# Optimization experiments

Hardware: AMD Instinct MI355X
Metric: run time of the kernel (lower is better)

Reference implementation:

```python
import jax, jax.numpy as jnp
import numpy as np

N_TREES = 10
N_DEPTH = 8
IN_DIM = 2048
CLASSES = 1000
BATCH = 16384
N_DECISION = 2 ** N_DEPTH - 1          # 255
N_LEAF = 2 ** (N_DEPTH + 1)            # 512 (module's own convention)


def _tiling_pattern():
    # Static gather pattern mapping each (leaf, depth) slot to an index into
    # the packed [decision_p, 1 - decision_p] tensor, exactly as in the source.
    tp = np.zeros((N_LEAF, N_DEPTH), dtype=np.int32)
    dec_idx = 0
    for n in range(N_DEPTH):
        j = 0
        for _ in range(2 ** n):
            rep = 2 ** (N_DEPTH - n)
            tp[j:j + rep, n] = dec_idx
            j += rep
            tp[j:j + rep, n] = N_DECISION + dec_idx
            j += rep
            dec_idx += 1
    return tp.reshape(-1)

FLAT_PATTERN = jnp.asarray(_tiling_pattern())  # [N_LEAF * N_DEPTH]


def setup_inputs() -> dict:
    key = jax.random.key(0)
    kx, kd, kl = jax.random.split(key, 3)
    x = jax.random.normal(kx, (BATCH, IN_DIM), dtype=jnp.float32)
    # small scale so sigmoid logits are not fully saturated (mimics uniform init)
    w_d = jax.random.normal(kd, (N_TREES, IN_DIM, N_DECISION), dtype=jnp.float32) * 0.02
    w_l = jax.random.normal(kl, (N_TREES, N_LEAF, CLASSES), dtype=jnp.float32)
    return {"x": x, "w_d": w_d, "w_l": w_l}


def reference(x, w_d, w_l):
    # decision probabilities for all trees: [T, B, N_DECISION]
    decision_p = jax.nn.sigmoid(jnp.einsum('bi,tid->tbd', x, w_d))
    # packed [p, 1-p]: [T, B, 2*N_DECISION]
    pack = jnp.concatenate([decision_p, 1.0 - decision_p], axis=-1)
    # static gather -> path probability factors: [T, B, N_LEAF, N_DEPTH]
    mu = pack[..., FLAT_PATTERN].reshape(N_TREES, x.shape[0], N_LEAF, N_DEPTH)
    leaf_prob = jnp.prod(mu, axis=-1)               # [T, B, N_LEAF]
    leaf_p = jax.nn.softmax(w_l, axis=-1)           # [T, N_LEAF, C]
    # sum over trees, then average
    return jnp.einsum('tbl,tlc->bc', leaf_prob, leaf_p) / N_TREES
```

## Files before the change

### kernel.cpp

```cpp
#include <hip/hip_runtime.h>
#include <stdint.h>

#define T_TREES 10
#define IN_DIM  2048
#define BATCH   16384
#define CLASSES 1000
#define NDEC    255
#define NPAD    256
#define K2DIM   (T_TREES * NPAD)
#define NPADC   1024

typedef unsigned short u16;
typedef float floatx4 __attribute__((ext_vector_type(4)));
typedef __bf16 bf16x8 __attribute__((ext_vector_type(8)));

__device__ __forceinline__ u16 f2bf(float f) {
    union { float f; uint32_t u; } v; v.f = f;
    uint32_t u = v.u;
    return (u16)((u + 0x7FFFu + ((u >> 16) & 1u)) >> 16);
}
__device__ __forceinline__ float bf2f(u16 h) {
    union { uint32_t u; float f; } v; v.u = ((uint32_t)h) << 16;
    return v.f;
}

__device__ __forceinline__ void gld16(u16* lds, const u16* g) {
    __builtin_amdgcn_global_load_lds(
        (__attribute__((address_space(1))) const void*)g,
        (__attribute__((address_space(3))) void*)lds,
        16, 0, 0);
}

__global__ __launch_bounds__(256) void cast_x_k(const float4* __restrict__ x,
                                                uint2* __restrict__ xb) {
    int i = blockIdx.x * 256 + threadIdx.x;
    float4 v = x[i];
    uint2 o;
    o.x = (uint32_t)f2bf(v.x) | ((uint32_t)f2bf(v.y) << 16);
    o.y = (uint32_t)f2bf(v.z) | ((uint32_t)f2bf(v.w) << 16);
    xb[i] = o;
}

__global__ void transpose_wd_k(const float* __restrict__ wd, u16* __restrict__ wdT) {
    __shared__ float tile[32][33];
    int tx = threadIdx.x, ty = threadIdx.y;
    int t = blockIdx.z;
    int i0 = blockIdx.x * 32, d0 = blockIdx.y * 32;
#pragma unroll
    for (int r = 0; r < 4; ++r) {
        int i = i0 + ty + r * 8;
        int d = d0 + tx;
        float v = (d < NDEC) ? wd[((size_t)t * IN_DIM + i) * NDEC + d] : 0.0f;
        tile[ty + r * 8][tx] = v;
    }
    __syncthreads();
#pragma unroll
    for (int r = 0; r < 4; ++r) {
        int dd = d0 + ty + r * 8;
        int ii = i0 + tx;
        wdT[((size_t)t * NPAD + dd) * IN_DIM + ii] = f2bf(tile[tx][ty + r * 8]);
    }
}

__global__ __launch_bounds__(256) void softmax_fold_k(const float* __restrict__ wl,
                                                      u16* __restrict__ B2) {
    int wid = threadIdx.x >> 6, lane = threadIdx.x & 63;
    int idx = blockIdx.x * 4 + wid;
    int t = idx >> 8, m = idx & 255;
    const float* r0 = wl + ((size_t)t * 512 + 2 * m) * CLASSES;
    const float* r1 = r0 + CLASSES;
    float v0[16], v1[16];
    float mx0 = -3.0e38f, mx1 = -3.0e38f;
#pragma unroll
    for (int j = 0; j < 16; ++j) {
        int c = lane + 64 * j;
        float a = (c < CLASSES) ? r0[c] : -3.0e38f;
        float b = (c < CLASSES) ? r1[c] : -3.0e38f;
        v0[j] = a; v1[j] = b;
        mx0 = fmaxf(mx0, a); mx1 = fmaxf(mx1, b);
    }
#pragma unroll
    for (int o = 32; o > 0; o >>= 1) {
        mx0 = fmaxf(mx0, __shfl_xor(mx0, o));
        mx1 = fmaxf(mx1, __shfl_xor(mx1, o));
    }
    float s0 = 0.f, s1 = 0.f;
#pragma unroll
    for (int j = 0; j < 16; ++j) {
        int c = lane + 64 * j;
        float e0 = (c < CLASSES) ? __expf(v0[j] - mx0) : 0.f;
        float e1 = (c < CLASSES) ? __expf(v1[j] - mx1) : 0.f;
        v0[j] = e0; v1[j] = e1; s0 += e0; s1 += e1;
    }
#pragma unroll
    for (int o = 32; o > 0; o >>= 1) { s0 += __shfl_xor(s0, o); s1 += __shfl_xor(s1, o); }
    float i0 = 0.1f / s0, i1 = 0.1f / s1;
#pragma unroll
    for (int j = 0; j < 16; ++j) {
        int c = lane + 64 * j;
        float v = (c < CLASSES) ? (v0[j] * i0 + v1[j] * i1) : 0.f;
        B2[(size_t)idx * NPADC + c] = f2bf(v);
    }
}

__global__ void transpose_b2_k(const u16* __restrict__ B2, u16* __restrict__ B2t) {
    __shared__ u16 tile[32][33];
    int tx = threadIdx.x, ty = threadIdx.y;
    int k0 = blockIdx.x * 32, c0 = blockIdx.y * 32;
#pragma unroll
    for (int r = 0; r < 4; ++r)
        tile[ty + r * 8][tx] = B2[(size_t)(k0 + ty + r * 8) * NPADC + c0 + tx];
    __syncthreads();
#pragma unroll
    for (int r = 0; r < 4; ++r)
        B2t[(size_t)(c0 + ty + r * 8) * K2DIM + k0 + tx] = tile[tx][ty + r * 8];
}

__global__ __launch_bounds__(256, 3) void gemm_bt(const u16* __restrict__ A,
                                                  const u16* __restrict__ B,
                                                  u16* __restrict__ Cout,
                                                  const int K, const long strideBz,
                                                  const long strideCz, const int ldc) {
    __shared__ __align__(16) u16 As[128 * 32];
    __shared__ __align__(16) u16 Bs[128 * 32];
    const int tid  = threadIdx.x;
    const int wid  = tid >> 6;
    const int lane = tid & 63;
    const int wr = wid >> 1, wc = wid & 1;
    const int quad = lane >> 4, t16 = lane & 15;

    const size_t m0 = (size_t)blockIdx.x * 128;
    const size_t n0 = (size_t)blockIdx.y * 128;
    const u16* Ag = A + m0 * (size_t)K;
    const u16* Bg = B + (size_t)blockIdx.z * strideBz + n0 * (size_t)K;

    const int ch0   = wid * 2;
    const int srow0 = ch0 * 16 + (lane >> 2);
    const int skk   = ((lane & 3) ^ ((lane >> 3) & 3)) * 8;
    const u16* ag0 = Ag + (size_t)srow0 * K + skk;
    const u16* ag1 = ag0 + (size_t)16 * K;
    const u16* bg0 = Bg + (size_t)srow0 * K + skk;
    const u16* bg1 = bg0 + (size_t)16 * K;
    u16* lA0 = &As[ch0 * 512];
    u16* lA1 = &As[ch0 * 512 + 512];
    u16* lB0 = &Bs[ch0 * 512];
    u16* lB1 = &Bs[ch0 * 512 + 512];
    const int sw = (quad ^ ((t16 >> 1) & 3)) * 8;

    floatx4 acc[4][4];
#pragma unroll
    for (int i = 0; i < 4; ++i)
#pragma unroll
        for (int j = 0; j < 4; ++j) acc[i][j] = (floatx4){0.f, 0.f, 0.f, 0.f};

    for (int k0 = 0; k0 < K; k0 += 32) {
        gld16(lA0, ag0 + k0);
        gld16(lA1, ag1 + k0);
        gld16(lB0, bg0 + k0);
        gld16(lB1, bg1 + k0);
        __syncthreads();

        bf16x8 af[4], bfr[4];
#pragma unroll
        for (int mi = 0; mi < 4; ++mi)
            af[mi] = *(const bf16x8*)&As[(wr * 64 + mi * 16 + t16) * 32 + sw];
#pragma unroll
        for (int ni = 0; ni < 4; ++ni)
            bfr[ni] = *(const bf16x8*)&Bs[(wc * 64 + ni * 16 + t16) * 32 + sw];
#pragma unroll
        for (int mi = 0; mi < 4; ++mi)
#pragma unroll
            for (int ni = 0; ni < 4; ++ni)
                acc[mi][ni] = __builtin_amdgcn_mfma_f32_16x16x32_bf16(
                    af[mi], bfr[ni], acc[mi][ni], 0, 0, 0);
        __syncthreads();
    }

    u16* C = Cout + (size_t)blockIdx.z * strideCz;
#pragma unroll
    for (int mi = 0; mi < 4; ++mi)
#pragma unroll
        for (int r = 0; r < 4; ++r) {
            size_t row = m0 + wr * 64 + mi * 16 + quad * 4 + r;
#pragma unroll
            for (int ni = 0; ni < 4; ++ni) {
                int col = (int)n0 + wc * 64 + ni * 16 + t16;
                float v = acc[mi][ni][r];
                float p = 1.0f / (1.0f + __expf(-v));
                C[row * (size_t)ldc + col] = f2bf(p);
            }
        }
}

__global__ __launch_bounds__(256, 2) void gemm2_k(const u16* __restrict__ A,
                                                  const u16* __restrict__ B,
                                                  float* __restrict__ C) {
    __shared__ __align__(16) u16 As[256 * 32];
    __shared__ __align__(16) u16 Bs[128 * 32];
    const int tid  = threadIdx.x;
    const int wid  = tid >> 6;
    const int lane = tid & 63;
    const int quad = lane >> 4, t16 = lane & 15;

    const size_t m0 = (size_t)blockIdx.x * 256;
    const size_t n0 = (size_t)blockIdx.y * 128;
    const u16* Ag = A + m0 * (size_t)K2DIM;
    const u16* Bg = B + n0 * (size_t)K2DIM;

    const int lrow = lane >> 2;
    const int skk  = ((lane & 3) ^ ((lane >> 3) & 3)) * 8;
    const u16* ag[4];
#pragma unroll
    for (int j = 0; j < 4; ++j)
        ag[j] = Ag + (size_t)((wid * 4 + j) * 16 + lrow) * K2DIM + skk;
    const u16* bg0 = Bg + (size_t)((wid * 2) * 16 + lrow) * K2DIM + skk;
    const u16* bg1 = bg0 + (size_t)16 * K2DIM;
    u16* lA = &As[wid * 4 * 512];
    u16* lB0 = &Bs[wid * 2 * 512];
    u16* lB1 = &Bs[wid * 2 * 512 + 512];
    const int sw = (quad ^ ((t16 >> 1) & 3)) * 8;

    floatx4 acc[4][8];
#pragma unroll
    for (int i = 0; i < 4; ++i)
#pragma unroll
        for (int j = 0; j < 8; ++j) acc[i][j] = (floatx4){0.f, 0.f, 0.f, 0.f};

    for (int k0 = 0; k0 < K2DIM; k0 += 32) {
#pragma unroll
        for (int j = 0; j < 4; ++j) gld16(lA + j * 512, ag[j] + k0);
        gld16(lB0, bg0 + k0);
        gld16(lB1, bg1 + k0);
        __syncthreads();

        bf16x8 af[4], bfr[8];
#pragma unroll
        for (int mi = 0; mi < 4; ++mi)
            af[mi] = *(const bf16x8*)&As[(wid * 64 + mi * 16 + t16) * 32 + sw];
#pragma unroll
        for (int ni = 0; ni < 8; ++ni)
            bfr[ni] = *(const bf16x8*)&Bs[(ni * 16 + t16) * 32 + sw];
#pragma unroll
        for (int mi = 0; mi < 4; ++mi)
#pragma unroll
            for (int ni = 0; ni < 8; ++ni)
                acc[mi][ni] = __builtin_amdgcn_mfma_f32_16x16x32_bf16(
                    af[mi], bfr[ni], acc[mi][ni], 0, 0, 0);
        __syncthreads();
    }

#pragma unroll
    for (int mi = 0; mi < 4; ++mi)
#pragma unroll
        for (int r = 0; r < 4; ++r) {
            size_t row = m0 + wid * 64 + mi * 16 + quad * 4 + r;
#pragma unroll
            for (int ni = 0; ni < 8; ++ni) {
                int col = (int)n0 + ni * 16 + t16;
                if (col < CLASSES) C[row * (size_t)CLASSES + col] = acc[mi][ni][r];
            }
        }
}

__global__ __launch_bounds__(256) void leafprod_k(const u16* __restrict__ dp,
                                                  u16* __restrict__ lp) {
    __shared__ float P[4][256];
    int wid = threadIdx.x >> 6, lane = threadIdx.x & 63;
    int idx = blockIdx.x * 4 + wid;
    int t = idx >> 14, b = idx & 16383;
    const u16* row = dp + (size_t)idx * NPAD;
#pragma unroll
    for (int j = 0; j < 4; ++j)
        P[wid][lane + 64 * j] = bf2f(row[lane + 64 * j]);
    __syncthreads();
#pragma unroll
    for (int j = 0; j < 4; ++j) {
        int m = lane + 64 * j;
        float prod = 1.0f;
#pragma unroll
        for (int n = 0; n < 8; ++n) {
            int dec  = (1 << n) - 1 + (m >> (8 - n));
            int side = (m >> (7 - n)) & 1;
            float p  = P[wid][dec];
            prod *= side ? (1.0f - p) : p;
        }
        lp[(size_t)b * K2DIM + t * NPAD + m] = f2bf(prod);
    }
}

extern "C" void kernel_launch(void* const* d_in, const int* in_sizes, int n_in,
                              void* d_out, int out_size, void* d_ws, size_t ws_size,
                              hipStream_t stream) {
    const float* x   = (const float*)d_in[0];
    const float* w_d = (const float*)d_in[1];
    const float* w_l = (const float*)d_in[2];
    float* out = (float*)d_out;

    char* w = (char*)d_ws;
    u16* B2t = (u16*)w;
    char* region = w + 5242880;
    u16* xb  = (u16*)region;
    u16* wdT = (u16*)(region + 67108864);
    u16* B2  = (u16*)(region + 67108864 + 10485760);
    u16* lp  = (u16*)region;
    u16* dp  = (u16*)(region + 83886080);

    cast_x_k<<<32768, 256, 0, stream>>>((const float4*)x, (uint2*)xb);
    transpose_wd_k<<<dim3(64, 8, T_TREES), dim3(32, 8), 0, stream>>>(w_d, wdT);
    softmax_fold_k<<<640, 256, 0, stream>>>(w_l, B2);
    transpose_b2_k<<<dim3(80, 32), dim3(32, 8), 0, stream>>>(B2, B2t);
    gemm_bt<<<dim3(128, 2, T_TREES), 256, 0, stream>>>(
        xb, wdT, dp, IN_DIM, (long)NPAD * IN_DIM, (long)BATCH * NPAD, NPAD);
    leafprod_k<<<40960, 256, 0, stream>>>(dp, lp);
    gemm2_k<<<dim3(64, 8), 256, 0, stream>>>(lp, B2t, out);
}
```

Baseline: 557.1 us.

## Replace both GEMMs with a software-pipelined 256x256 8-wave MFMA kernel

Both GEMMs now use one templated 512-thread kernel with 256x256 tiles and a BK=64 slab. Global-to-LDS loads are staged two tiles ahead through an 8-slot LDS ring, with explicit vmcnt/lgkmcnt waits, sched barriers and setprio so MFMA work overlaps loads. The first GEMM is no longer batched per tree; it treats the concatenated tree dimension as N and writes dp in a [B, T*256] layout, and leafprod's indexing is changed to match. This is meant to remove the single-buffered sync-per-k-step stalls and raise data reuse per tile, at the cost of high register and LDS use, hand-tuned wait counts that are easy to get wrong, and fewer blocks in flight.

```diff
diff --git a/kernel.cpp b/kernel.cpp
--- a/kernel.cpp
+++ b/kernel.cpp
@@ -24,10 +24,10 @@
     return v.f;
 }
 
-__device__ __forceinline__ void gld16(u16* lds, const u16* g) {
+__device__ __forceinline__ void gld16(u16* lds_p, const u16* g) {
     __builtin_amdgcn_global_load_lds(
         (__attribute__((address_space(1))) const void*)g,
-        (__attribute__((address_space(3))) void*)lds,
+        (__attribute__((address_space(3))) void*)lds_p,
         16, 0, 0);
 }
 
@@ -116,150 +116,166 @@
         B2t[(size_t)(c0 + ty + r * 8) * K2DIM + k0 + tx] = tile[tx][ty + r * 8];
 }
 
-__global__ __launch_bounds__(256, 3) void gemm_bt(const u16* __restrict__ A,
-                                                  const u16* __restrict__ B,
-                                                  u16* __restrict__ Cout,
-                                                  const int K, const long strideBz,
-                                                  const long strideCz, const int ldc) {
-    __shared__ __align__(16) u16 As[128 * 32];
-    __shared__ __align__(16) u16 Bs[128 * 32];
+
+#define WAITLGKM_(n) asm volatile("s_waitcnt lgkmcnt(" #n ")" ::: "memory")
+#define WAITLGKM(n) WAITLGKM_(n)
+#define WAITVM_(n) asm volatile("s_waitcnt vmcnt(" #n ")" ::: "memory")
+#define WAITVM(n) WAITVM_(n)
+#define SB  __builtin_amdgcn_sched_barrier(0)
+#define BAR __builtin_amdgcn_s_barrier()
+
+template<int NT, int EPI>
+__global__ __launch_bounds__(512, 2) void gemm8p(const u16* __restrict__ A,
+                                                 const u16* __restrict__ B,
+                                                 void* __restrict__ Cout) {
+    constexpr int K = NT * 64;
+    __shared__ __align__(16) u16 lds[8 * 8192];
+
     const int tid  = threadIdx.x;
     const int wid  = tid >> 6;
     const int lane = tid & 63;
-    const int wr = wid >> 1, wc = wid & 1;
+    const int wm = wid >> 2, wn = wid & 3;
     const int quad = lane >> 4, t16 = lane & 15;
 
-    const size_t m0 = (size_t)blockIdx.x * 128;
-    const size_t n0 = (size_t)blockIdx.y * 128;
-    const u16* Ag = A + m0 * (size_t)K;
-    const u16* Bg = B + (size_t)blockIdx.z * strideBz + n0 * (size_t)K;
-
-    const int ch0   = wid * 2;
-    const int srow0 = ch0 * 16 + (lane >> 2);
-    const int skk   = ((lane & 3) ^ ((lane >> 3) & 3)) * 8;
-    const u16* ag0 = Ag + (size_t)srow0 * K + skk;
-    const u16* ag1 = ag0 + (size_t)16 * K;
-    const u16* bg0 = Bg + (size_t)srow0 * K + skk;
-    const u16* bg1 = bg0 + (size_t)16 * K;
-    u16* lA0 = &As[ch0 * 512];
-    u16* lA1 = &As[ch0 * 512 + 512];
-    u16* lB0 = &Bs[ch0 * 512];
-    u16* lB1 = &Bs[ch0 * 512 + 512];
-    const int sw = (quad ^ ((t16 >> 1) & 3)) * 8;
-
-    floatx4 acc[4][4];
-#pragma unroll
-    for (int i = 0; i < 4; ++i)
+    const size_t m0 = (size_t)blockIdx.x * 256;
+    const size_t n0 = (size_t)blockIdx.y * 256;
+    const u16* __restrict__ Ag = A + m0 * (size_t)K;
+    const u16* __restrict__ Bg = B + n0 * (size_t)K;
+
+    const uint32_t stOff = (uint32_t)((wid * 8 + (lane >> 3)) * K)
+                         + (uint32_t)(((lane & 7) ^ ((lane >> 3) & 7)) * 8);
+    const uint32_t stLds = (uint32_t)(wid * 8 * 64);
+
+#define STAGE(slot, o, tk) do { \
+    const u16* gp_ = (((o) < 2) ? Bg : Ag) + ((size_t)(((o) & 1) * 128) * K) \
+                   + ((size_t)(tk) * 64) + stOff; \
+    gld16(&lds[(slot) * 8192 + stLds], gp_); \
+    gld16(&lds[(slot) * 8192 + stLds + 4096], gp_ + (size_t)64 * K); \
+  } while (0)
+
+#define AOFF(P, mi, kk) (((P) * 4 + 2 + wm) * 8192 + ((mi) * 16 + t16) * 64 \
+                         + ((((kk) * 4 + quad) ^ (t16 & 7)) * 8))
+#define BOFF(P, ni, kk) (((P) * 4 + ((wn * 64 + (ni) * 16) >> 7)) * 8192 \
+                         + (((wn * 64 + (ni) * 16) & 127) + t16) * 64 \
+                         + ((((kk) * 4 + quad) ^ (t16 & 7)) * 8))
+
+#define RD2(dst, P, mi0) do { \
+    dst[0][0] = *(const bf16x8*)&lds[AOFF(P, (mi0),     0)]; \
+    dst[0][1] = *(const bf16x8*)&lds[AOFF(P, (mi0),     1)]; \
+    dst[1][0] = *(const bf16x8*)&lds[AOFF(P, (mi0) + 1, 0)]; \
+    dst[1][1] = *(const bf16x8*)&lds[AOFF(P, (mi0) + 1, 1)]; \
+  } while (0)
+
+#define RDB(dst, P) do { \
+    _Pragma("unroll") \
+    for (int ni_ = 0; ni_ < 4; ++ni_) { \
+      dst[ni_][0] = *(const bf16x8*)&lds[BOFF(P, ni_, 0)]; \
+      dst[ni_][1] = *(const bf16x8*)&lds[BOFF(P, ni_, 1)]; \
+    } \
+  } while (0)
+
+#define MFQ(p, aq, bs) do { \
+    _Pragma("unroll") \
+    for (int kk_ = 0; kk_ < 2; ++kk_) { \
+      _Pragma("unroll") \
+      for (int ni_ = 0; ni_ < 4; ++ni_) { \
+        acc[2*(p)][ni_]   = __builtin_amdgcn_mfma_f32_16x16x32_bf16( \
+            aq[0][kk_], bs[ni_][kk_], acc[2*(p)][ni_], 0, 0, 0); \
+        acc[2*(p)+1][ni_] = __builtin_amdgcn_mfma_f32_16x16x32_bf16( \
+            aq[1][kk_], bs[ni_][kk_], acc[2*(p)+1][ni_], 0, 0, 0); \
+      } \
+    } \
+  } while (0)
+
+    floatx4 acc[8][4];
+#pragma unroll
+    for (int i = 0; i < 8; ++i)
 #pragma unroll
         for (int j = 0; j < 4; ++j) acc[i][j] = (floatx4){0.f, 0.f, 0.f, 0.f};
 
-    for (int k0 = 0; k0 < K; k0 += 32) {
-        gld16(lA0, ag0 + k0);
-        gld16(lA1, ag1 + k0);
-        gld16(lB0, bg0 + k0);
-        gld16(lB1, bg1 + k0);
-        __syncthreads();
-
-        bf16x8 af[4], bfr[4];
-#pragma unroll
-        for (int mi = 0; mi < 4; ++mi)
-            af[mi] = *(const bf16x8*)&As[(wr * 64 + mi * 16 + t16) * 32 + sw];
-#pragma unroll
-        for (int ni = 0; ni < 4; ++ni)
-            bfr[ni] = *(const bf16x8*)&Bs[(wc * 64 + ni * 16 + t16) * 32 + sw];
-#pragma unroll
-        for (int mi = 0; mi < 4; ++mi)
-#pragma unroll
-            for (int ni = 0; ni < 4; ++ni)
-                acc[mi][ni] = __builtin_amdgcn_mfma_f32_16x16x32_bf16(
-                    af[mi], bfr[ni], acc[mi][ni], 0, 0, 0);
-        __syncthreads();
-    }
-
-    u16* C = Cout + (size_t)blockIdx.z * strideCz;
-#pragma unroll
-    for (int mi = 0; mi < 4; ++mi)
-#pragma unroll
-        for (int r = 0; r < 4; ++r) {
-            size_t row = m0 + wr * 64 + mi * 16 + quad * 4 + r;
-#pragma unroll
-            for (int ni = 0; ni < 4; ++ni) {
-                int col = (int)n0 + wc * 64 + ni * 16 + t16;
-                float v = acc[mi][ni][r];
-                float p = 1.0f / (1.0f + __expf(-v));
-                C[row * (size_t)ldc + col] = f2bf(p);
+    bf16x8 bA[4][2], bB[4][2];
+    bf16x8 a0A[2][2], a0B[2][2];
+    bf16x8 aT1[2][2], aT2[2][2], aT3[2][2];
+
+    STAGE(0, 0, 0); STAGE(1, 1, 0); STAGE(2, 2, 0); STAGE(3, 3, 0);
+    STAGE(4, 0, 1); STAGE(5, 1, 1); STAGE(6, 2, 1);
+    WAITVM(6);
+    BAR; SB;
+    RDB(bA, 0); RD2(a0A, 0, 0);
+
+#define TILE(P, t, S_A1, S_T2, NEXTF, VMN, bcur, bnxt, a0c, a0n) do { \
+     \
+    RD2(aT1, P, 2); \
+    if (S_A1) { STAGE((1 - (P)) * 4 + 3, 3, (t) + 1); } \
+    WAITLGKM(4); SB; \
+    __builtin_amdgcn_s_setprio(1); MFQ(0, a0c, bcur); __builtin_amdgcn_s_setprio(0); \
+    BAR; SB; \
+     \
+    RD2(aT2, P, 4); RD2(aT3, P, 6); \
+    if (S_T2) { STAGE((P) * 4 + 0, 0, (t) + 2); } \
+    WAITLGKM(8); SB; \
+    __builtin_amdgcn_s_setprio(1); MFQ(1, aT1, bcur); __builtin_amdgcn_s_setprio(0); \
+    BAR; SB; \
+     \
+    if (S_T2) { STAGE((P) * 4 + 1, 1, (t) + 2); } \
+    WAITLGKM(0); SB; \
+    __builtin_amdgcn_s_setprio(1); MFQ(2, aT2, bcur); __builtin_amdgcn_s_setprio(0); \
+    BAR; SB; \
+     \
+    if (S_T2) { STAGE((P) * 4 + 2, 2, (t) + 2); } \
+    if (NEXTF) { WAITVM(VMN); } \
+    BAR; SB; \
+    if (NEXTF) { RDB(bnxt, 1 - (P)); RD2(a0n, 1 - (P), 0); SB; } \
+    __builtin_amdgcn_s_setprio(1); MFQ(3, aT3, bcur); __builtin_amdgcn_s_setprio(0); \
+    BAR; SB; \
+  } while (0)
+
+    int t = 0;
+#pragma unroll 1
+    for (int it = 0; it < NT / 2 - 1; ++it, t += 2) {
+        TILE(0, t,     true, true, true, 6, bA, bB, a0A, a0B);
+        TILE(1, t + 1, true, true, true, 6, bB, bA, a0B, a0A);
+    }
+    TILE(0, t,     true,  false, true,  0, bA, bB, a0A, a0B);
+    TILE(1, t + 1, false, false, false, 0, bB, bA, a0B, a0A);
+
+    if constexpr (EPI == 0) {
+        u16* C = (u16*)Cout;
+#pragma unroll
+        for (int mi = 0; mi < 8; ++mi)
+#pragma unroll
+            for (int r = 0; r < 4; ++r) {
+                const size_t row = m0 + wm * 128 + mi * 16 + quad * 4 + r;
+#pragma unroll
+                for (int ni = 0; ni < 4; ++ni) {
+                    const int col = (int)n0 + wn * 64 + ni * 16 + t16;
+                    float v = acc[mi][ni][r];
+                    float p = 1.0f / (1.0f + __expf(-v));
+                    C[row * (size_t)K2DIM + col] = f2bf(p);
+                }
             }
-        }
-}
-
-__global__ __launch_bounds__(256, 2) void gemm2_k(const u16* __restrict__ A,
-                                                  const u16* __restrict__ B,
-                                                  float* __restrict__ C) {
-    __shared__ __align__(16) u16 As[256 * 32];
-    __shared__ __align__(16) u16 Bs[128 * 32];
-    const int tid  = threadIdx.x;
-    const int wid  = tid >> 6;
-    const int lane = tid & 63;
-    const int quad = lane >> 4, t16 = lane & 15;
-
-    const size_t m0 = (size_t)blockIdx.x * 256;
-    const size_t n0 = (size_t)blockIdx.y * 128;
-    const u16* Ag = A + m0 * (size_t)K2DIM;
-    const u16* Bg = B + n0 * (size_t)K2DIM;
-
-    const int lrow = lane >> 2;
-    const int skk  = ((lane & 3) ^ ((lane >> 3) & 3)) * 8;
-    const u16* ag[4];
-#pragma unroll
-    for (int j = 0; j < 4; ++j)
-        ag[j] = Ag + (size_t)((wid * 4 + j) * 16 + lrow) * K2DIM + skk;
-    const u16* bg0 = Bg + (size_t)((wid * 2) * 16 + lrow) * K2DIM + skk;
-    const u16* bg1 = bg0 + (size_t)16 * K2DIM;
-    u16* lA = &As[wid * 4 * 512];
-    u16* lB0 = &Bs[wid * 2 * 512];
-    u16* lB1 = &Bs[wid * 2 * 512 + 512];
-    const int sw = (quad ^ ((t16 >> 1) & 3)) * 8;
-
-    floatx4 acc[4][8];
-#pragma unroll
-    for (int i = 0; i < 4; ++i)
-#pragma unroll
-        for (int j = 0; j < 8; ++j) acc[i][j] = (floatx4){0.f, 0.f, 0.f, 0.f};
-
-    for (int k0 = 0; k0 < K2DIM; k0 += 32) {
-#pragma unroll
-        for (int j = 0; j < 4; ++j) gld16(lA + j * 512, ag[j] + k0);
-        gld16(lB0, bg0 + k0);
-        gld16(lB1, bg1 + k0);
-        __syncthreads();
-
-        bf16x8 af[4], bfr[8];
-#pragma unroll
-        for (int mi = 0; mi < 4; ++mi)
-            af[mi] = *(const bf16x8*)&As[(wid * 64 + mi * 16 + t16) * 32 + sw];
-#pragma unroll
-        for (int ni = 0; ni < 8; ++ni)
-            bfr[ni] = *(const bf16x8*)&Bs[(ni * 16 + t16) * 32 + sw];
-#pragma unroll
-        for (int mi = 0; mi < 4; ++mi)
-#pragma unroll
-            for (int ni = 0; ni < 8; ++ni)
-                acc[mi][ni] = __builtin_amdgcn_mfma_f32_16x16x32_bf16(
-                    af[mi], bfr[ni], acc[mi][ni], 0, 0, 0);
-        __syncthreads();
-    }
-
-#pragma unroll
-    for (int mi = 0; mi < 4; ++mi)
-#pragma unroll
-        for (int r = 0; r < 4; ++r) {
-            size_t row = m0 + wid * 64 + mi * 16 + quad * 4 + r;
-#pragma unroll
-            for (int ni = 0; ni < 8; ++ni) {
-                int col = (int)n0 + ni * 16 + t16;
-                if (col < CLASSES) C[row * (size_t)CLASSES + col] = acc[mi][ni][r];
+    } else {
+        float* C = (float*)Cout;
+#pragma unroll
+        for (int mi = 0; mi < 8; ++mi)
+#pragma unroll
+            for (int r = 0; r < 4; ++r) {
+                const size_t row = m0 + wm * 128 + mi * 16 + quad * 4 + r;
+#pragma unroll
+                for (int ni = 0; ni < 4; ++ni) {
+                    const int col = (int)n0 + wn * 64 + ni * 16 + t16;
+                    if (col < CLASSES)
+                        C[row * (size_t)CLASSES + col] = acc[mi][ni][r];
+                }
             }
-        }
+    }
+#undef TILE
+#undef MFQ
+#undef RDB
+#undef RD2
+#undef BOFF
+#undef AOFF
+#undef STAGE
 }
 
 __global__ __launch_bounds__(256) void leafprod_k(const u16* __restrict__ dp,
@@ -268,7 +284,7 @@
     int wid = threadIdx.x >> 6, lane = threadIdx.x & 63;
     int idx = blockIdx.x * 4 + wid;
     int t = idx >> 14, b = idx & 16383;
-    const u16* row = dp + (size_t)idx * NPAD;
+    const u16* row = dp + (size_t)b * K2DIM + t * NPAD;
 #pragma unroll
     for (int j = 0; j < 4; ++j)
         P[wid][lane + 64 * j] = bf2f(row[lane + 64 * j]);
@@ -309,8 +325,7 @@
     transpose_wd_k<<<dim3(64, 8, T_TREES), dim3(32, 8), 0, stream>>>(w_d, wdT);
     softmax_fold_k<<<640, 256, 0, stream>>>(w_l, B2);
     transpose_b2_k<<<dim3(80, 32), dim3(32, 8), 0, stream>>>(B2, B2t);
-    gemm_bt<<<dim3(128, 2, T_TREES), 256, 0, stream>>>(
-        xb, wdT, dp, IN_DIM, (long)NPAD * IN_DIM, (long)BATCH * NPAD, NPAD);
+    gemm8p<32, 0><<<dim3(64, 10), 512, 0, stream>>>(xb, wdT, dp);
     leafprod_k<<<40960, 256, 0, stream>>>(dp, lp);
-    gemm2_k<<<dim3(64, 8), 256, 0, stream>>>(lp, B2t, out);
-}
+    gemm8p<40, 1><<<dim3(64, 4), 512, 0, stream>>>(lp, B2t, out);
+}
```

After: 570.6 us. 2.4% more time.
